# Optimization experiments

Measured on AMD Instinct MI355X. Metric: run time of the kernel, lower is better.

Reference implementation:

```python
import jax, jax.numpy as jnp
import numpy as np

B, N, C = 8, 1024, 768
H = 12
HD = C // H
STAGES = 3
MLP_H = 4 * C
EPS = 1e-5


def _layernorm(x, w, b):
    mu = jnp.mean(x, axis=-1, keepdims=True)
    var = jnp.mean(jnp.square(x - mu), axis=-1, keepdims=True)
    return (x - mu) * jax.lax.rsqrt(var + EPS) * w + b


def setup_inputs() -> dict:
    key = jax.random.key(0)
    ks = jax.random.split(key, 16)
    s = 0.02
    return {
        "x": jax.random.normal(ks[0], (B, N, C), dtype=jnp.float32),
        # stacked per-stage attention params (torch Linear layout: [out, in])
        "qkv_w": jax.random.normal(ks[1], (STAGES, 3 * C, C), dtype=jnp.float32) * s,
        "proj_w": jax.random.normal(ks[2], (STAGES, C, C), dtype=jnp.float32) * s,
        "proj_b": jnp.zeros((STAGES, C), dtype=jnp.float32),
        "ln1_w": jnp.ones((C,), dtype=jnp.float32),
        "ln1_b": jnp.zeros((C,), dtype=jnp.float32),
        "ln2_w": jnp.ones((C,), dtype=jnp.float32),
        "ln2_b": jnp.zeros((C,), dtype=jnp.float32),
        "mlp_w1": jax.random.normal(ks[3], (MLP_H, C), dtype=jnp.float32) * s,
        "mlp_b1": jnp.zeros((MLP_H,), dtype=jnp.float32),
        "mlp_w2": jax.random.normal(ks[4], (C, MLP_H), dtype=jnp.float32) * s,
        "mlp_b2": jnp.zeros((C,), dtype=jnp.float32),
        "focus_w": jnp.ones((STAGES,), dtype=jnp.float32),
    }


def reference(x, qkv_w, proj_w, proj_b, ln1_w, ln1_b, ln2_w, ln2_b,
              mlp_w1, mlp_b1, mlp_w2, mlp_b2, focus_w):
    scale = HD ** -0.5
    h = _layernorm(x, ln1_w, ln1_b)  # shared norm1(x) input to all stages
    attn_out = jnp.zeros_like(x)
    for i in range(STAGES):
        qkv = jnp.einsum('bnc,oc->bno', h, qkv_w[i])  # [B,N,3C], no bias (qkv_bias=False)
        qkv = qkv.reshape(B, N, 3, H, HD).transpose(2, 0, 3, 1, 4)  # [3,B,H,N,HD]
        q, k, v = qkv[0], qkv[1], qkv[2]
        attn = jax.nn.softmax(jnp.einsum('bhnd,bhmd->bhnm', q, k) * scale, axis=-1)
        o = jnp.einsum('bhnm,bhmd->bhnd', attn, v)  # [B,H,N,HD]
        o = o.transpose(0, 2, 1, 3).reshape(B, N, C)
        o = jnp.einsum('bnc,oc->bno', o, proj_w[i]) + proj_b[i]
        attn_out = attn_out + focus_w[i] * o
    x = x + attn_out
    h2 = _layernorm(x, ln2_w, ln2_b)
    h2 = jax.nn.gelu(jnp.einsum('bnc,hc->bnh', h2, mlp_w1) + mlp_b1, approximate=False)
    mlp_out = jnp.einsum('bnh,ch->bnc', h2, mlp_w2) + mlp_b2
    return x + mlp_out
```

## Files before the change

### kernel.cpp

```cpp
#include <hip/hip_runtime.h>
#include <hip/hip_bf16.h>
#include <math.h>

#define B_    8
#define N_    1024
#define C_    768
#define H_    12
#define HD_   64
#define MLPH_ 3072
#define M_ROWS 8192
#define QKV3  6912
#define PK    2304

typedef float  f32x4   __attribute__((ext_vector_type(4)));
typedef float  f32x16  __attribute__((ext_vector_type(16)));
typedef __bf16 bf16x8  __attribute__((ext_vector_type(8)));

__device__ __forceinline__ f32x4 mfma16(bf16x8 a, bf16x8 b, f32x4 c) {
    return __builtin_amdgcn_mfma_f32_16x16x32_bf16(a, b, c, 0, 0, 0);
}
__device__ __forceinline__ f32x16 mfma32(bf16x8 a, bf16x8 b, f32x16 c) {
    return __builtin_amdgcn_mfma_f32_32x32x16_bf16(a, b, c, 0, 0, 0);
}

__device__ __forceinline__ unsigned packbf(float a, float b) {
    __bf16 x = (__bf16)a, y = (__bf16)b;
    union { __bf16 h; unsigned short u; } ux, uy;
    ux.h = x; uy.h = y;
    return (unsigned)ux.u | ((unsigned)uy.u << 16);
}

__global__ __launch_bounds__(256) void cast_f32_bf16(const float* __restrict__ in,
                                                     __bf16* __restrict__ out, int n) {
    int i = blockIdx.x * 256 + threadIdx.x;
    if (i < n) out[i] = (__bf16)in[i];
}

__global__ __launch_bounds__(256) void prep_proj_w(const float* __restrict__ pw,
                                                   const float* __restrict__ focus,
                                                   __bf16* __restrict__ out) {
    int i = blockIdx.x * 256 + threadIdx.x;
    int c = i % C_;
    int s = (i / C_) % 3;
    int o = i / PK;
    out[i] = (__bf16)(focus[s] * pw[((size_t)s * C_ + o) * C_ + c]);
}

__global__ __launch_bounds__(256) void ln_to_bf16(const float* __restrict__ x,
                                                  const float* __restrict__ g,
                                                  const float* __restrict__ bta,
                                                  __bf16* __restrict__ out) {
    int row = blockIdx.x;
    const float* xr = x + (size_t)row * C_;
    int t = threadIdx.x;
    float v0 = xr[t], v1 = xr[t + 256], v2 = xr[t + 512];
    float s  = v0 + v1 + v2;
    float s2 = v0 * v0 + v1 * v1 + v2 * v2;
#pragma unroll
    for (int m = 1; m < 64; m <<= 1) { s += __shfl_xor(s, m); s2 += __shfl_xor(s2, m); }
    __shared__ float red[8];
    int w = t >> 6, lane = t & 63;
    if (lane == 0) { red[w] = s; red[4 + w] = s2; }
    __syncthreads();
    s  = red[0] + red[1] + red[2] + red[3];
    s2 = red[4] + red[5] + red[6] + red[7];
    float mu   = s * (1.f / C_);
    float var  = s2 * (1.f / C_) - mu * mu;
    float rstd = rsqrtf(var + 1e-5f);
    __bf16* orow = out + (size_t)row * C_;
    orow[t]       = (__bf16)((v0 - mu) * rstd * g[t]       + bta[t]);
    orow[t + 256] = (__bf16)((v1 - mu) * rstd * g[t + 256] + bta[t + 256]);
    orow[t + 512] = (__bf16)((v2 - mu) * rstd * g[t + 512] + bta[t + 512]);
}

template <int MODE>
__global__ __launch_bounds__(256) void gemm_bt(
    const __bf16* __restrict__ A, const __bf16* __restrict__ W,
    int M, int N, int K,
    __bf16* __restrict__ obf, float* __restrict__ of32,
    const float* __restrict__ resid, const float* __restrict__ bias,
    const float* __restrict__ focus_p)
{
    __shared__ __bf16 As[128][40];
    __shared__ __bf16 Bs[128][40];

    const int t    = threadIdx.x;
    const int lane = t & 63;
    const int w    = t >> 6;
    const int wr   = w >> 1, wc = w & 1;
    const int m0   = blockIdx.y * 128, n0 = blockIdx.x * 128;
    const int lo   = lane & 15;
    const int lk8  = (lane >> 4) * 8;

    const int r0 = t >> 2;
    const int cb = (t & 3) * 8;

    f32x4 acc[4][4] = {};

    int4 ra0, ra1, rb0, rb1;
    auto load_tile = [&](int k0) {
        ra0 = *(const int4*)&A[(size_t)(m0 + r0)      * K + k0 + cb];
        ra1 = *(const int4*)&A[(size_t)(m0 + r0 + 64) * K + k0 + cb];
        rb0 = *(const int4*)&W[(size_t)(n0 + r0)      * K + k0 + cb];
        rb1 = *(const int4*)&W[(size_t)(n0 + r0 + 64) * K + k0 + cb];
    };
    load_tile(0);

    for (int k0 = 0; k0 < K; k0 += 32) {
        __syncthreads();
        *(int4*)&As[r0][cb]      = ra0;
        *(int4*)&As[r0 + 64][cb] = ra1;
        *(int4*)&Bs[r0][cb]      = rb0;
        *(int4*)&Bs[r0 + 64][cb] = rb1;
        __syncthreads();
        if (k0 + 32 < K) load_tile(k0 + 32);

        bf16x8 af[4], bfr[4];
#pragma unroll
        for (int mi = 0; mi < 4; mi++) af[mi]  = *(const bf16x8*)&As[wr * 64 + mi * 16 + lo][lk8];
#pragma unroll
        for (int ni = 0; ni < 4; ni++) bfr[ni] = *(const bf16x8*)&Bs[wc * 64 + ni * 16 + lo][lk8];
#pragma unroll
        for (int mi = 0; mi < 4; mi++)
#pragma unroll
            for (int ni = 0; ni < 4; ni++)
                acc[mi][ni] = mfma16(af[mi], bfr[ni], acc[mi][ni]);
    }

    float f0 = 0.f, f1 = 0.f, f2 = 0.f;
    if (MODE == 1) { f0 = focus_p[0]; f1 = focus_p[1]; f2 = focus_p[2]; }

#pragma unroll
    for (int mi = 0; mi < 4; mi++) {
#pragma unroll
        for (int ni = 0; ni < 4; ni++) {
            int col = n0 + wc * 64 + ni * 16 + lo;
#pragma unroll
            for (int r = 0; r < 4; r++) {
                int row = m0 + wr * 64 + mi * 16 + (lane >> 4) * 4 + r;
                size_t o = (size_t)row * N + col;
                float v = acc[mi][ni][r];
                if (MODE == 0) {
                    obf[o] = (__bf16)v;
                } else if (MODE == 1) {
                    float be = f0 * bias[col] + f1 * bias[col + C_] + f2 * bias[col + 2 * C_];
                    of32[o] = resid[o] + v + be;
                } else if (MODE == 2) {
                    float u = v + bias[col];
                    float ge = 0.5f * u * (1.0f + erff(u * 0.70710678118654752f));
                    obf[o] = (__bf16)ge;
                } else {
                    of32[o] = resid[o] + v + bias[col];
                }
            }
        }
    }
}

__global__ __launch_bounds__(256) void attn_kernel(const __bf16* __restrict__ qkv,
                                                   __bf16* __restrict__ obuf) {
    const int bid  = blockIdx.x;
    const int idx  = bid >> 3;
    const int grp  = (bid & 7) * 36 + (idx >> 3);
    const int qt   = idx & 7;
    const int s    = grp / 96;
    const int rem  = grp % 96;
    const int b    = rem / 12;
    const int h    = rem % 12;
    const int q0   = qt * 128;

    const int t = threadIdx.x, lane = t & 63, w = t >> 6;
    const int l31 = lane & 31, hi1 = lane >> 5;

    __shared__ __bf16 Kf[4096];
    __shared__ __bf16 Vf[4096];
    __shared__ float  Lsm[128];

    const size_t rs = QKV3;
    const __bf16* qb = qkv + (size_t)b * N_ * rs + (size_t)s * PK + h * HD_;
    const __bf16* kb = qb + C_;
    const __bf16* vb = qb + 2 * C_;

    bf16x8 aq[4];
#pragma unroll
    for (int dk = 0; dk < 4; dk++)
        aq[dk] = *(const bf16x8*)(qb + (size_t)(q0 + w * 32 + l31) * rs + dk * 16 + hi1 * 8);

    f32x16 oacc[2] = {};
    float lsum = 0.f;

    int4 kreg[2]; uint4 vreg[2];
    auto load_tile = [&](int k0) {
#pragma unroll
        for (int p = 0; p < 2; p++) {
            int id = p * 256 + t;
            int kr = id >> 3, d0 = (id & 7) * 8;
            kreg[p] = *(const int4*)(kb + (size_t)(k0 + kr) * rs + d0);
            int kr2 = id & 63, d2 = ((id >> 6) * 8);
            vreg[p] = *(const uint4*)(vb + (size_t)(k0 + kr2) * rs + d2);
        }
    };
    load_tile(0);

    const float cexp = 0.18033688011112042f;

    for (int kt = 0; kt < 16; kt++) {
        __syncthreads();
#pragma unroll
        for (int p = 0; p < 2; p++) {
            int id = p * 256 + t;
            int chunk = (id & 7) * 64 + (id >> 3);
            int c = chunk ^ (id & 7);
            *(int4*)&Kf[c * 8] = kreg[p];
        }
        {
            int k8 = lane >> 3, par = lane & 1, koff = lane & 6;
#pragma unroll
            for (int p = 0; p < 2; p++) {
                int d2 = ((p * 256 + t) >> 6) * 8;
#pragma unroll
                for (int i = 0; i < 4; i++) {
                    unsigned mw = vreg[p][i];
                    unsigned pw = (unsigned)__builtin_amdgcn_mov_dpp((int)mw, 0xB1, 0xF, 0xF, true);
                    unsigned out = par ? ((pw >> 16) | (mw & 0xFFFF0000u))
                                       : ((mw & 0xFFFFu) | (pw << 16));
                    int d = d2 + 2 * i + par;
                    int chunk = k8 * 64 + d;
                    int c = chunk ^ k8;
                    *(unsigned*)&Vf[c * 8 + koff] = out;
                }
            }
        }
        __syncthreads();
        if (kt < 15) load_tile((kt + 1) * 64);

        f32x16 sacc[2] = {};
#pragma unroll
        for (int ks = 0; ks < 2; ks++)
#pragma unroll
            for (int dk = 0; dk < 4; dk++) {
                int d8 = dk * 2 + hi1;
                int c = (d8 * 64 + ks * 32 + l31) ^ d8;
                bf16x8 kf = *(const bf16x8*)&Kf[c * 8];
                sacc[ks] = mfma32(kf, aq[dk], sacc[ks]);
            }

#pragma unroll
        for (int ks = 0; ks < 2; ks++) {
            float pe[16];
#pragma unroll
            for (int r = 0; r < 16; r++) {
                pe[r] = exp2f(sacc[ks][r] * cexp);
                lsum += pe[r];
            }
            unsigned pk[8];
#pragma unroll
            for (int i = 0; i < 8; i++) pk[i] = packbf(pe[2 * i], pe[2 * i + 1]);

            unsigned a0 = pk[0], a2 = pk[2], a1 = pk[1], a3 = pk[3];
            {
                auto r0 = __builtin_amdgcn_permlane32_swap((int)a0, (int)a2, false, false);
                a0 = (unsigned)r0[0]; a2 = (unsigned)r0[1];
                auto r1 = __builtin_amdgcn_permlane32_swap((int)a1, (int)a3, false, false);
                a1 = (unsigned)r1[0]; a3 = (unsigned)r1[1];
            }
            unsigned b0 = pk[4], b2 = pk[6], b1 = pk[5], b3 = pk[7];
            {
                auto r0 = __builtin_amdgcn_permlane32_swap((int)b0, (int)b2, false, false);
                b0 = (unsigned)r0[0]; b2 = (unsigned)r0[1];
                auto r1 = __builtin_amdgcn_permlane32_swap((int)b1, (int)b3, false, false);
                b1 = (unsigned)r1[0]; b3 = (unsigned)r1[1];
            }
            union { unsigned u[4]; bf16x8 v; } fr0, fr1;
            fr0.u[0] = a0; fr0.u[1] = a1; fr0.u[2] = a2; fr0.u[3] = a3;
            fr1.u[0] = b0; fr1.u[1] = b1; fr1.u[2] = b2; fr1.u[3] = b3;

#pragma unroll
            for (int f = 0; f < 2; f++) {
                bf16x8 pa = f ? fr1.v : fr0.v;
#pragma unroll
                for (int dh = 0; dh < 2; dh++) {
                    int k8 = ks * 4 + f * 2 + hi1;
                    int c = (k8 * 64 + dh * 32 + l31) ^ k8;
                    bf16x8 vf = *(const bf16x8*)&Vf[c * 8];
                    oacc[dh] = mfma32(pa, vf, oacc[dh]);
                }
            }
        }
    }

    float ls2 = lsum + __shfl_xor(lsum, 32);
    if (lane < 32) Lsm[w * 32 + lane] = ls2;
    f32x4 Ls[4];
#pragma unroll
    for (int g = 0; g < 4; g++)
        Ls[g] = *(const f32x4*)&Lsm[w * 32 + 8 * g + 4 * hi1];

    __bf16* obase = obuf + ((size_t)b * N_ + q0 + w * 32) * PK + (size_t)s * C_ + h * HD_ + l31;
#pragma unroll
    for (int g = 0; g < 4; g++)
#pragma unroll
        for (int i = 0; i < 4; i++) {
            float inv = 1.0f / Ls[g][i];
            int q_local = i + 8 * g + 4 * hi1;
            __bf16* orow = obase + (size_t)q_local * PK;
            orow[0]  = (__bf16)(oacc[0][4 * g + i] * inv);
            orow[32] = (__bf16)(oacc[1][4 * g + i] * inv);
        }
}

extern "C" void kernel_launch(void* const* d_in, const int* in_sizes, int n_in,
                              void* d_out, int out_size, void* d_ws, size_t ws_size,
                              hipStream_t stream) {
    const float* x      = (const float*)d_in[0];
    const float* qkv_w  = (const float*)d_in[1];
    const float* proj_w = (const float*)d_in[2];
    const float* proj_b = (const float*)d_in[3];
    const float* ln1_w  = (const float*)d_in[4];
    const float* ln1_b  = (const float*)d_in[5];
    const float* ln2_w  = (const float*)d_in[6];
    const float* ln2_b  = (const float*)d_in[7];
    const float* mlp_w1 = (const float*)d_in[8];
    const float* mlp_b1 = (const float*)d_in[9];
    const float* mlp_w2 = (const float*)d_in[10];
    const float* mlp_b2 = (const float*)d_in[11];
    const float* focus  = (const float*)d_in[12];
    float* out = (float*)d_out;

    char* ws = (char*)d_ws;
    size_t off = 0;
    auto alloc = [&](size_t bytes) {
        char* p = ws + off;
        off += (bytes + 255) & ~(size_t)255;
        return p;
    };
    __bf16* h1   = (__bf16*)alloc((size_t)M_ROWS * C_ * 2);
    __bf16* qkvb = (__bf16*)alloc((size_t)M_ROWS * QKV3 * 2);
    __bf16* ob   = (__bf16*)alloc((size_t)M_ROWS * PK * 2);
    float*  x1   = (float*) alloc((size_t)M_ROWS * C_ * 4);
    __bf16* wq   = (__bf16*)alloc((size_t)QKV3 * C_ * 2);
    __bf16* wp   = (__bf16*)alloc((size_t)C_ * PK * 2);
    __bf16* w1   = (__bf16*)alloc((size_t)MLPH_ * C_ * 2);
    __bf16* w2   = (__bf16*)alloc((size_t)C_ * MLPH_ * 2);
    if (off > ws_size) return;
    __bf16* h2  = h1;
    __bf16* hid = qkvb;

    const int nq = QKV3 * C_;
    const int np = C_ * PK;
    const int n1 = MLPH_ * C_;
    cast_f32_bf16<<<(nq + 255) / 256, 256, 0, stream>>>(qkv_w, wq, nq);
    prep_proj_w<<<(np + 255) / 256, 256, 0, stream>>>(proj_w, focus, wp);
    cast_f32_bf16<<<(n1 + 255) / 256, 256, 0, stream>>>(mlp_w1, w1, n1);
    cast_f32_bf16<<<(n1 + 255) / 256, 256, 0, stream>>>(mlp_w2, w2, n1);

    ln_to_bf16<<<M_ROWS, 256, 0, stream>>>(x, ln1_w, ln1_b, h1);

    gemm_bt<0><<<dim3(QKV3 / 128, M_ROWS / 128), 256, 0, stream>>>(
        h1, wq, M_ROWS, QKV3, C_, qkvb, nullptr, nullptr, nullptr, nullptr);

    attn_kernel<<<3 * B_ * H_ * (N_ / 128), 256, 0, stream>>>(qkvb, ob);

    gemm_bt<1><<<dim3(C_ / 128, M_ROWS / 128), 256, 0, stream>>>(
        ob, wp, M_ROWS, C_, PK, nullptr, x1, x, proj_b, focus);

    ln_to_bf16<<<M_ROWS, 256, 0, stream>>>(x1, ln2_w, ln2_b, h2);

    gemm_bt<2><<<dim3(MLPH_ / 128, M_ROWS / 128), 256, 0, stream>>>(
        h2, w1, M_ROWS, MLPH_, C_, hid, nullptr, nullptr, mlp_b1, nullptr);
    gemm_bt<3><<<dim3(C_ / 128, M_ROWS / 128), 256, 0, stream>>>(
        hid, w2, M_ROWS, C_, MLPH_, nullptr, out, x1, mlp_b2, nullptr);
}
```

Before: 528.2 us.

## Double-buffer GEMM tiles via direct global-to-LDS loads; MFMA row sums in attention

The GEMM now streams A and W tiles straight into double-buffered shared memory with global_load_lds, so the next K-slice is fetched while the current one is multiplied. This removes the register round-trip and one barrier per iteration. The row padding is gone, so LDS bank conflicts on fragment reads may increase. Separately, the attention kernel computes softmax denominators with an extra MFMA against a ones vector instead of scalar adds, a shuffle and shared-memory exchange. That also makes the sum use the bf16-rounded probabilities, consistent with the PV product.

```diff
diff --git a/kernel.cpp b/kernel.cpp
--- a/kernel.cpp
+++ b/kernel.cpp
@@ -21,6 +21,13 @@
 }
 __device__ __forceinline__ f32x16 mfma32(bf16x8 a, bf16x8 b, f32x16 c) {
     return __builtin_amdgcn_mfma_f32_32x32x16_bf16(a, b, c, 0, 0, 0);
+}
+
+__device__ __forceinline__ void gl16(const __bf16* g, __bf16* l) {
+    __builtin_amdgcn_global_load_lds(
+        (const __attribute__((address_space(1))) unsigned int*)g,
+        (__attribute__((address_space(3))) unsigned int*)l,
+        16, 0, 0);
 }
 
 __device__ __forceinline__ unsigned packbf(float a, float b) {
@@ -81,8 +88,8 @@
     const float* __restrict__ resid, const float* __restrict__ bias,
     const float* __restrict__ focus_p)
 {
-    __shared__ __bf16 As[128][40];
-    __shared__ __bf16 Bs[128][40];
+    __shared__ __bf16 As[2][128][32];
+    __shared__ __bf16 Bs[2][128][32];
 
     const int t    = threadIdx.x;
     const int lane = t & 63;
@@ -92,39 +99,46 @@
     const int lo   = lane & 15;
     const int lk8  = (lane >> 4) * 8;
 
-    const int r0 = t >> 2;
-    const int cb = (t & 3) * 8;
+    const int srow = lane >> 2;
+    const int scol = (lane & 3) * 8;
+
+    auto stage = [&](int buf, int k0) {
+#pragma unroll
+        for (int i = 0; i < 2; i++) {
+            const int chunk = w * 2 + i;
+            const int row   = chunk * 16 + srow;
+            gl16(&A[(size_t)(m0 + row) * K + k0 + scol], &As[buf][chunk * 16][0]);
+            gl16(&W[(size_t)(n0 + row) * K + k0 + scol], &Bs[buf][chunk * 16][0]);
+        }
+    };
 
     f32x4 acc[4][4] = {};
 
-    int4 ra0, ra1, rb0, rb1;
-    auto load_tile = [&](int k0) {
-        ra0 = *(const int4*)&A[(size_t)(m0 + r0)      * K + k0 + cb];
-        ra1 = *(const int4*)&A[(size_t)(m0 + r0 + 64) * K + k0 + cb];
-        rb0 = *(const int4*)&W[(size_t)(n0 + r0)      * K + k0 + cb];
-        rb1 = *(const int4*)&W[(size_t)(n0 + r0 + 64) * K + k0 + cb];
-    };
-    load_tile(0);
-
-    for (int k0 = 0; k0 < K; k0 += 32) {
-        __syncthreads();
-        *(int4*)&As[r0][cb]      = ra0;
-        *(int4*)&As[r0 + 64][cb] = ra1;
-        *(int4*)&Bs[r0][cb]      = rb0;
-        *(int4*)&Bs[r0 + 64][cb] = rb1;
-        __syncthreads();
-        if (k0 + 32 < K) load_tile(k0 + 32);
+    stage(0, 0);
+    asm volatile("s_waitcnt vmcnt(0)" ::: "memory");
+    __syncthreads();
+
+    int cur = 0;
+    for (int k0 = 0;;) {
+        const int nk = k0 + 32;
+        if (nk < K) stage(cur ^ 1, nk);
 
         bf16x8 af[4], bfr[4];
 #pragma unroll
-        for (int mi = 0; mi < 4; mi++) af[mi]  = *(const bf16x8*)&As[wr * 64 + mi * 16 + lo][lk8];
-#pragma unroll
-        for (int ni = 0; ni < 4; ni++) bfr[ni] = *(const bf16x8*)&Bs[wc * 64 + ni * 16 + lo][lk8];
+        for (int mi = 0; mi < 4; mi++) af[mi]  = *(const bf16x8*)&As[cur][wr * 64 + mi * 16 + lo][lk8];
+#pragma unroll
+        for (int ni = 0; ni < 4; ni++) bfr[ni] = *(const bf16x8*)&Bs[cur][wc * 64 + ni * 16 + lo][lk8];
 #pragma unroll
         for (int mi = 0; mi < 4; mi++)
 #pragma unroll
             for (int ni = 0; ni < 4; ni++)
                 acc[mi][ni] = mfma16(af[mi], bfr[ni], acc[mi][ni]);
+
+        k0 = nk;
+        if (k0 >= K) break;
+        asm volatile("s_waitcnt vmcnt(0)" ::: "memory");
+        __syncthreads();
+        cur ^= 1;
     }
 
     float f0 = 0.f, f1 = 0.f, f2 = 0.f;
@@ -174,7 +188,6 @@
 
     __shared__ __bf16 Kf[4096];
     __shared__ __bf16 Vf[4096];
-    __shared__ float  Lsm[128];
 
     const size_t rs = QKV3;
     const __bf16* qb = qkv + (size_t)b * N_ * rs + (size_t)s * PK + h * HD_;
@@ -186,8 +199,12 @@
     for (int dk = 0; dk < 4; dk++)
         aq[dk] = *(const bf16x8*)(qb + (size_t)(q0 + w * 32 + l31) * rs + dk * 16 + hi1 * 8);
 
+    bf16x8 ones;
+#pragma unroll
+    for (int j = 0; j < 8; j++) ones[j] = (__bf16)1.0f;
+
     f32x16 oacc[2] = {};
-    float lsum = 0.f;
+    f32x16 lacc = {};
 
     int4 kreg[2]; uint4 vreg[2];
     auto load_tile = [&](int k0) {
@@ -249,10 +266,8 @@
         for (int ks = 0; ks < 2; ks++) {
             float pe[16];
 #pragma unroll
-            for (int r = 0; r < 16; r++) {
+            for (int r = 0; r < 16; r++)
                 pe[r] = exp2f(sacc[ks][r] * cexp);
-                lsum += pe[r];
-            }
             unsigned pk[8];
 #pragma unroll
             for (int i = 0; i < 8; i++) pk[i] = packbf(pe[2 * i], pe[2 * i + 1]);
@@ -285,23 +300,17 @@
                     bf16x8 vf = *(const bf16x8*)&Vf[c * 8];
                     oacc[dh] = mfma32(pa, vf, oacc[dh]);
                 }
+                lacc = mfma32(pa, ones, lacc);
             }
         }
     }
 
-    float ls2 = lsum + __shfl_xor(lsum, 32);
-    if (lane < 32) Lsm[w * 32 + lane] = ls2;
-    f32x4 Ls[4];
+    __bf16* obase = obuf + ((size_t)b * N_ + q0 + w * 32) * PK + (size_t)s * C_ + h * HD_ + l31;
 #pragma unroll
     for (int g = 0; g < 4; g++)
-        Ls[g] = *(const f32x4*)&Lsm[w * 32 + 8 * g + 4 * hi1];
-
-    __bf16* obase = obuf + ((size_t)b * N_ + q0 + w * 32) * PK + (size_t)s * C_ + h * HD_ + l31;
-#pragma unroll
-    for (int g = 0; g < 4; g++)
 #pragma unroll
         for (int i = 0; i < 4; i++) {
-            float inv = 1.0f / Ls[g][i];
+            float inv = 1.0f / lacc[4 * g + i];
             int q_local = i + 8 * g + 4 * hi1;
             __bf16* orow = obase + (size_t)q_local * PK;
             orow[0]  = (__bf16)(oacc[0][4 * g + i] * inv);
```

New measurement: 662.6 us. 25.4% more time.
